# Kernel optimization log

Measured on AMD Instinct MI355X. Metric: run time of the kernel, lower is better.

Reference implementation:

```python
import jax, jax.numpy as jnp
import numpy as np

# dims: H heads, D=word_size (d_model), E=embed_dim per head, N=seq_len=n, K=linformer k
H, D, E, N, K = 16, 1024, 64, 4096, 256


def setup_inputs() -> dict:
    key = jax.random.key(0)
    ks = jax.random.split(key, 9)
    s = 0.02  # init scale for weights
    return {
        "x":  jax.random.normal(ks[0], (N, D), jnp.float32),
        # per-head QKV linears: torch Linear weight is (out=E, in=D), bias (E,)
        "Wq": jax.random.normal(ks[1], (H, E, D), jnp.float32) * s,
        "bq": jnp.zeros((H, E), jnp.float32),
        "Wk": jax.random.normal(ks[2], (H, E, D), jnp.float32) * s,
        "bk": jnp.zeros((H, E), jnp.float32),
        "Wv": jax.random.normal(ks[3], (H, E, D), jnp.float32) * s,
        "bv": jnp.zeros((H, E), jnp.float32),
        # per-head E/F sequence projections: Linear(n=N, k=K) -> weight (K, N), bias (K,)
        "Ew": jax.random.normal(ks[4], (H, K, N), jnp.float32) * s,
        "Eb": jnp.zeros((H, K), jnp.float32),
        "Fw": jax.random.normal(ks[5], (H, K, N), jnp.float32) * s,
        "Fb": jnp.zeros((H, K), jnp.float32),
        # output projection: Linear(H*E, E, bias=False) -> weight (E, H*E)
        "Wo": jax.random.normal(ks[6], (E, H * E), jnp.float32) * s,
    }


def reference(x, Wq, bq, Wk, bk, Wv, bv, Ew, Eb, Fw, Fb, Wo):
    # per-head Q/K/V projections, batched over heads: (H, N, E)
    q = jnp.einsum('nd,hed->hne', x, Wq) + bq[:, None, :]
    k = jnp.einsum('nd,hed->hne', x, Wk) + bk[:, None, :]
    v = jnp.einsum('nd,hed->hne', x, Wv) + bv[:, None, :]
    # low-rank sequence-length projection of K and V: (H, K, E)
    kp = jnp.einsum('hjn,hne->hje', Ew, k) + Eb[:, :, None]
    vp = jnp.einsum('hjn,hne->hje', Fw, v) + Fb[:, :, None]
    # scaled dot-product attention against projected keys: (H, N, K)
    score = jnp.einsum('hne,hje->hnj', q, kp) / jnp.sqrt(jnp.float32(E))
    attn = jax.nn.softmax(score, axis=-1)
    z = jnp.einsum('hnj,hje->hne', attn, vp)  # (H, N, E)
    # concat heads along feature dim (matches torch.cat(dim=1)): (N, H*E)
    zs = jnp.transpose(z, (1, 0, 2)).reshape(N, H * E)
    # final projection Linear(H*E, E, bias=False)
    return zs @ Wo.T  # (N, E)
```

## Files before the change

### kernel.cpp

```cpp
#include <hip/hip_runtime.h>
#include <hip/hip_bf16.h>

typedef __attribute__((ext_vector_type(4))) float f32x4;
typedef __attribute__((ext_vector_type(8))) short s16x8;
typedef __attribute__((ext_vector_type(4))) short s16x4;
typedef unsigned short u16;


__device__ __forceinline__ f32x4 mfma16(s16x8 a, s16x8 b, f32x4 c) {
    return __builtin_amdgcn_mfma_f32_16x16x32_bf16(a, b, c, 0, 0, 0);
}

__device__ __forceinline__ u16 bf(float f) {
    union { float f; unsigned u; } x; x.f = f;
    return (u16)((x.u + 0x7fffu + ((x.u >> 16) & 1u)) >> 16);
}
__device__ __forceinline__ unsigned pkbf(float a, float b) {
    union { float f; unsigned u; } x, y; x.f = a; y.f = b;
    unsigned ra = x.u + 0x7fffu + ((x.u >> 16) & 1u);
    unsigned rb = y.u + 0x7fffu + ((y.u >> 16) & 1u);
    return (ra >> 16) | (rb & 0xffff0000u);
}

__device__ __forceinline__ void gl_lds16(const u16* g, u16* l) {
    __builtin_amdgcn_global_load_lds(
        (const __attribute__((address_space(1))) unsigned*)g,
        (__attribute__((address_space(3))) unsigned*)l, 16, 0, 0);
}


__global__ __launch_bounds__(256) void cvt_all_kernel(
        const float* __restrict__ x,  const float* __restrict__ Wq,
        const float* __restrict__ Wk, const float* __restrict__ Wv,
        const float* __restrict__ Wo,
        u16* __restrict__ xb, u16* __restrict__ wb, u16* __restrict__ wob) {
    int i = blockIdx.x * 256 + threadIdx.x;
    const float* src; u16* dst; int off;
    if (i < 1048576)      { src = x;  dst = xb;            off = i; }
    else if (i < 1310720) { src = Wq; dst = wb;            off = i - 1048576; }
    else if (i < 1572864) { src = Wk; dst = wb + 1048576;  off = i - 1310720; }
    else if (i < 1835008) { src = Wv; dst = wb + 2097152;  off = i - 1572864; }
    else if (i < 1851392) { src = Wo; dst = wob;           off = i - 1835008; }
    else return;
    f32x4 v = ((const f32x4*)src)[off];
    union { s16x4 v; unsigned u[2]; } r;
    r.u[0] = pkbf(v.x, v.y);
    r.u[1] = pkbf(v.z, v.w);
    ((s16x4*)dst)[off] = r.v;
}


__global__ __launch_bounds__(256, 3) void qkv_kernel(
        const u16* __restrict__ xb, const u16* __restrict__ wb,
        const float* __restrict__ bq, const float* __restrict__ bk,
        const float* __restrict__ bv,
        u16* __restrict__ qo, u16* __restrict__ kTo, u16* __restrict__ vTo) {
    __shared__ u16 As[128 * 32];
    __shared__ u16 Bs[128 * 32];
    int bx   = blockIdx.x % 24;
    int by   = blockIdx.x / 24;
    int tid  = threadIdx.x;
    int lane = tid & 63, w = tid >> 6;
    int l15  = lane & 15, quad = lane >> 4;
    int wr   = w >> 1, wc = w & 1;

    const u16* Ag = xb + (size_t)(by * 128 + (tid >> 2)) * 1024 + (tid & 3) * 8;
    const u16* Bg = wb + (size_t)(bx * 128 + (tid >> 2)) * 1024 + (tid & 3) * 8;
    u16* Al = As + tid * 8;
    u16* Bl = Bs + tid * 8;

    const u16* abase = As + (wr * 64 + l15) * 32 + quad * 8;
    const u16* bbase = Bs + (wc * 64 + l15) * 32 + quad * 8;

    f32x4 acc[4][4] = {};
    for (int k0 = 0; k0 < 1024; k0 += 32) {
        gl_lds16(Ag + k0, Al);
        gl_lds16(Ag + 64 * 1024 + k0, Al + 64 * 32);
        gl_lds16(Bg + k0, Bl);
        gl_lds16(Bg + 64 * 1024 + k0, Bl + 64 * 32);
        __syncthreads();
        s16x8 a[4], b[4];
#pragma unroll
        for (int mi = 0; mi < 4; mi++) a[mi] = *(const s16x8*)(abase + mi * 16 * 32);
#pragma unroll
        for (int nj = 0; nj < 4; nj++) b[nj] = *(const s16x8*)(bbase + nj * 16 * 32);
#pragma unroll
        for (int mi = 0; mi < 4; mi++)
#pragma unroll
            for (int nj = 0; nj < 4; nj++) acc[mi][nj] = mfma16(a[mi], b[nj], acc[mi][nj]);
        __syncthreads();
    }

    int fblk = (bx * 128 + wc * 64) >> 6;
    int mat  = fblk >> 4, h = fblk & 15;
    const float* bias = (mat == 0) ? bq : (mat == 1 ? bk : bv);
#pragma unroll
    for (int nj = 0; nj < 4; nj++) {
        int e = nj * 16 + l15;
        float bb = bias[h * 64 + e];
#pragma unroll
        for (int mi = 0; mi < 4; mi++) {
            int n0 = by * 128 + wr * 64 + mi * 16 + quad * 4;
            f32x4 c = acc[mi][nj];
            if (mat == 0) {
                u16* p = qo + ((size_t)h * 4096 + n0) * 64 + e;
#pragma unroll
                for (int r = 0; r < 4; r++) p[(size_t)r * 64] = bf(c[r] + bb);
            } else {
                u16* p = (mat == 1 ? kTo : vTo) + ((size_t)h * 64 + e) * 4096 + n0;
                union { s16x4 v; u16 s[4]; } pk;
#pragma unroll
                for (int r = 0; r < 4; r++) pk.s[r] = bf(c[r] + bb);
                *(s16x4*)p = pk.v;
            }
        }
    }
}


__global__ __launch_bounds__(256, 2) void kpvp_kernel(
        const float* __restrict__ Ew, const float* __restrict__ Fw,
        const u16* __restrict__ kT, const u16* __restrict__ vT,
        float* __restrict__ accs) {
    __shared__ u16 As[256 * 40];
    __shared__ u16 Bs[64 * 32];
    int b    = blockIdx.x;
    int ks   = b & 15, h = (b >> 4) & 15, p = b >> 8;
    int tid  = threadIdx.x;
    int lane = tid & 63, w = tid >> 6;
    int l15  = lane & 15, quad = lane >> 4;

    const float* Ag = (p ? Fw : Ew)
        + (size_t)(h * 256 + (tid >> 3)) * 4096 + ks * 256 + (tid & 7) * 4;
    const u16* Bg = (p ? vT : kT)
        + ((size_t)h * 64 + (tid >> 2)) * 4096 + ks * 256 + (tid & 3) * 8;
    u16* Aw = As + (tid >> 3) * 40 + (tid & 7) * 4;
    u16* Bl = Bs + tid * 8;

    const u16* abase = As + (w * 64 + l15) * 40 + quad * 8;
    const u16* bbase = Bs + l15 * 32 + quad * 8;

    f32x4 acc[4][4] = {};
    for (int s = 0; s < 8; s++) {
        int kk = s * 32;
        gl_lds16(Bg + kk, Bl);
#pragma unroll
        for (int pr = 0; pr < 8; pr++) {
            f32x4 v = *(const f32x4*)(Ag + (size_t)pr * 32 * 4096 + kk);
            union { s16x4 q; unsigned u[2]; } rr;
            rr.u[0] = pkbf(v.x, v.y);
            rr.u[1] = pkbf(v.z, v.w);
            *(s16x4*)(Aw + pr * 32 * 40) = rr.q;
        }
        __syncthreads();
        s16x8 a[4], bb2[4];
#pragma unroll
        for (int mt = 0; mt < 4; mt++) a[mt] = *(const s16x8*)(abase + mt * 16 * 40);
#pragma unroll
        for (int nt = 0; nt < 4; nt++) bb2[nt] = *(const s16x8*)(bbase + nt * 16 * 32);
#pragma unroll
        for (int mt = 0; mt < 4; mt++)
#pragma unroll
            for (int nt = 0; nt < 4; nt++)
                acc[mt][nt] = mfma16(a[mt], bb2[nt], acc[mt][nt]);
        __syncthreads();
    }

    size_t base = (size_t)ks * 524288
        + ((size_t)(p * 16 + h) * 256 + w * 64 + quad * 4) * 64 + l15;
#pragma unroll
    for (int mt = 0; mt < 4; mt++)
#pragma unroll
        for (int nt = 0; nt < 4; nt++)
#pragma unroll
            for (int r = 0; r < 4; r++)
                accs[base + (size_t)(mt * 16 + r) * 64 + nt * 16] = acc[mt][nt][r];
}


__global__ __launch_bounds__(256) void packkv_kernel(
        const float* __restrict__ accs, const float* __restrict__ Eb,
        const float* __restrict__ Fb, u16* __restrict__ kp, u16* __restrict__ vpT) {
    int idx = blockIdx.x * 256 + threadIdx.x;
    float v = 0.f;
#pragma unroll
    for (int s = 0; s < 16; s++) v += accs[idx + (size_t)s * 524288];
    int p = idx >> 18, h = (idx >> 14) & 15, j = (idx >> 6) & 255, e = idx & 63;
    if (p == 0) {
        v += Eb[h * 256 + j];
        kp[((size_t)(h * 256 + j)) * 64 + e] = bf(v * 0.125f);
    } else {
        v += Fb[h * 256 + j];
        vpT[((size_t)(h * 64 + e)) * 256 + j] = bf(v);
    }
}


__global__ __launch_bounds__(256) void attn_kernel(
        const u16* __restrict__ q, const u16* __restrict__ kp,
        const u16* __restrict__ vpT, u16* __restrict__ zs) {
    __shared__ u16 ps[4][16][256];
    int bm   = blockIdx.x & 63, h = blockIdx.x >> 6;
    int lane = threadIdx.x & 63, w = threadIdx.x >> 6;
    int l15  = lane & 15, quad = lane >> 4;
    int nbase = bm * 64 + w * 16;

    f32x4 s[16] = {};
    const u16* qp  = q  + ((size_t)h * 4096 + nbase + l15) * 64 + quad * 8;
    const u16* kpp = kp + ((size_t)h * 256 + l15) * 64 + quad * 8;
#pragma unroll
    for (int e0 = 0; e0 < 64; e0 += 32) {
        s16x8 a = *(const s16x8*)(qp + e0);
#pragma unroll
        for (int jt = 0; jt < 16; jt++) {
            s16x8 b = *(const s16x8*)(kpp + jt * 16 * 64 + e0);
            s[jt] = mfma16(a, b, s[jt]);
        }
    }

    float lsum[4];
#pragma unroll
    for (int r = 0; r < 4; r++) {
        float m = s[0][r];
#pragma unroll
        for (int jt = 1; jt < 16; jt++) m = fmaxf(m, s[jt][r]);
        m = fmaxf(m, __shfl_xor(m, 1));
        m = fmaxf(m, __shfl_xor(m, 2));
        m = fmaxf(m, __shfl_xor(m, 4));
        m = fmaxf(m, __shfl_xor(m, 8));
        float l = 0.f;
#pragma unroll
        for (int jt = 0; jt < 16; jt++) {
            float pv = __expf(s[jt][r] - m);
            s[jt][r] = pv;
            l += pv;
        }
        l += __shfl_xor(l, 1);
        l += __shfl_xor(l, 2);
        l += __shfl_xor(l, 4);
        l += __shfl_xor(l, 8);
        lsum[r] = l;
    }

#pragma unroll
    for (int jt = 0; jt < 16; jt++)
#pragma unroll
        for (int r = 0; r < 4; r++)
            ps[w][quad * 4 + r][jt * 16 + l15] = bf(s[jt][r]);
    __syncthreads();

    f32x4 z[4] = {};
    const u16* vp = vpT + ((size_t)h * 64 + l15) * 256 + quad * 8;
#pragma unroll
    for (int kj = 0; kj < 8; kj++) {
        s16x8 a = *(const s16x8*)&ps[w][l15][kj * 32 + quad * 8];
#pragma unroll
        for (int et = 0; et < 4; et++) {
            s16x8 b = *(const s16x8*)(vp + et * 16 * 256 + kj * 32);
            z[et] = mfma16(a, b, z[et]);
        }
    }
#pragma unroll
    for (int et = 0; et < 4; et++) {
        int e = et * 16 + l15;
        u16* o = zs + ((size_t)(nbase + quad * 4)) * 1024 + h * 64 + e;
#pragma unroll
        for (int r = 0; r < 4; r++) o[(size_t)r * 1024] = bf(z[et][r] / lsum[r]);
    }
}


__global__ __launch_bounds__(256) void out_kernel(
        const u16* __restrict__ zs, const u16* __restrict__ wob,
        float* __restrict__ oslice) {
    int ks   = blockIdx.x & 3;
    int bm   = blockIdx.x >> 2;
    int lane = threadIdx.x & 63, w = threadIdx.x >> 6;
    int l15  = lane & 15, quad = lane >> 4;
    int row0 = bm * 128 + w * 32;

    const u16* A = zs  + (size_t)(row0 + l15) * 1024 + ks * 256 + quad * 8;
    const u16* B = wob + (size_t)l15 * 1024 + ks * 256 + quad * 8;

    f32x4 acc[2][4] = {};
    for (int k = 0; k < 256; k += 32) {
        s16x8 a0 = *(const s16x8*)(A + k);
        s16x8 a1 = *(const s16x8*)(A + 16 * 1024 + k);
#pragma unroll
        for (int nt = 0; nt < 4; nt++) {
            s16x8 bv = *(const s16x8*)(B + (size_t)nt * 16 * 1024 + k);
            acc[0][nt] = mfma16(a0, bv, acc[0][nt]);
            acc[1][nt] = mfma16(a1, bv, acc[1][nt]);
        }
    }
    float* os = oslice + (size_t)ks * 262144;
#pragma unroll
    for (int mt = 0; mt < 2; mt++)
#pragma unroll
        for (int nt = 0; nt < 4; nt++) {
            int e = nt * 16 + l15;
            int n0 = row0 + mt * 16 + quad * 4;
            float* o = os + (size_t)n0 * 64 + e;
#pragma unroll
            for (int r = 0; r < 4; r++) o[(size_t)r * 64] = acc[mt][nt][r];
        }
}

__global__ __launch_bounds__(256) void outred_kernel(
        const float* __restrict__ oslice, float* __restrict__ out) {
    int i = blockIdx.x * 256 + threadIdx.x;
    out[i] = oslice[i] + oslice[i + 262144] + oslice[i + 524288] + oslice[i + 786432];
}


extern "C" void kernel_launch(void* const* d_in, const int* in_sizes, int n_in,
                              void* d_out, int out_size, void* d_ws, size_t ws_size,
                              hipStream_t stream) {
    const float* x  = (const float*)d_in[0];
    const float* Wq = (const float*)d_in[1];
    const float* bq = (const float*)d_in[2];
    const float* Wk = (const float*)d_in[3];
    const float* bk = (const float*)d_in[4];
    const float* Wv = (const float*)d_in[5];
    const float* bv = (const float*)d_in[6];
    const float* Ew = (const float*)d_in[7];
    const float* Eb = (const float*)d_in[8];
    const float* Fw = (const float*)d_in[9];
    const float* Fb = (const float*)d_in[10];
    const float* Wo = (const float*)d_in[11];

    char* ws = (char*)d_ws;
    u16*   qb   = (u16*)(ws + 0);
    u16*   kT   = (u16*)(ws + 8388608);
    u16*   vT   = (u16*)(ws + 16777216);
    u16*   zsb  = (u16*)(ws + 25165824);
    float* accs = (float*)(ws + 33554432);
    u16*   kp   = (u16*)(ws + 67108864);
    u16*   vpT  = (u16*)(ws + 67633152);
    u16*   xb   = (u16*)(ws + 68157440);
    u16*   wb   = (u16*)(ws + 76546048);
    u16*   wob  = (u16*)(ws + 82837504);

    cvt_all_kernel<<<7232, 256, 0, stream>>>(x, Wq, Wk, Wv, Wo, xb, wb, wob);
    qkv_kernel<<<768, 256, 0, stream>>>(xb, wb, bq, bk, bv, qb, kT, vT);
    kpvp_kernel<<<512, 256, 0, stream>>>(Ew, Fw, kT, vT, accs);
    packkv_kernel<<<2048, 256, 0, stream>>>(accs, Eb, Fb, kp, vpT);
    attn_kernel<<<1024, 256, 0, stream>>>(qb, kp, vpT, zsb);
    out_kernel<<<128, 256, 0, stream>>>(zsb, wob, (float*)accs);
    outred_kernel<<<1024, 256, 0, stream>>>((const float*)accs, (float*)d_out);
}
```

Baseline: 299.4 us.

## Retile kpvp into two launches, vectorize packkv, keep attention probs in registers

The kpvp GEMM now covers half of the K rows per block, with a 2x2 wave layout and a higher occupancy bound, and is split into two launches over the split-K halves. packkv now reads vectorized fp32 partials and transposes vp through LDS so its stores are coalesced. The attention kernel swaps the MFMA operand order so each lane holds a full score column. The softmax reduction then needs only cross-quad shuffles, and the bf16 probabilities feed a K=16 MFMA straight from registers with no LDS round-trip. The normalization moves before the PV product, which shifts where bf16 rounding happens, and the extra launch adds some overhead.

```diff
diff --git a/kernel.cpp b/kernel.cpp
--- a/kernel.cpp
+++ b/kernel.cpp
@@ -9,6 +9,16 @@
 
 __device__ __forceinline__ f32x4 mfma16(s16x8 a, s16x8 b, f32x4 c) {
     return __builtin_amdgcn_mfma_f32_16x16x32_bf16(a, b, c, 0, 0, 0);
+}
+
+__device__ __forceinline__ f32x4 mfma_k16(s16x4 a, s16x4 b, f32x4 c) {
+#if __has_builtin(__builtin_amdgcn_mfma_f32_16x16x16bf16_1k)
+    return __builtin_amdgcn_mfma_f32_16x16x16bf16_1k(a, b, c, 0, 0, 0);
+#else
+    s16x8 a8 = { a[0], a[1], a[2], a[3], 0, 0, 0, 0 };
+    s16x8 b8 = { b[0], b[1], b[2], b[3], 0, 0, 0, 0 };
+    return __builtin_amdgcn_mfma_f32_16x16x32_bf16(a8, b8, c, 0, 0, 0);
+#endif
 }
 
 __device__ __forceinline__ u16 bf(float f) {
@@ -118,34 +128,35 @@
 }
 
 
-__global__ __launch_bounds__(256, 2) void kpvp_kernel(
+__global__ __launch_bounds__(256, 4) void kpvp_kernel(
         const float* __restrict__ Ew, const float* __restrict__ Fw,
         const u16* __restrict__ kT, const u16* __restrict__ vT,
-        float* __restrict__ accs) {
-    __shared__ u16 As[256 * 40];
+        float* __restrict__ accs, int ks0) {
+    __shared__ u16 As[128 * 40];
     __shared__ u16 Bs[64 * 32];
     int b    = blockIdx.x;
-    int ks   = b & 15, h = (b >> 4) & 15, p = b >> 8;
+    int ks   = (b & 7) + ks0, jt = (b >> 3) & 1, h = (b >> 4) & 15, p = b >> 8;
     int tid  = threadIdx.x;
     int lane = tid & 63, w = tid >> 6;
     int l15  = lane & 15, quad = lane >> 4;
+    int wm   = w & 1, wn = w >> 1;
 
     const float* Ag = (p ? Fw : Ew)
-        + (size_t)(h * 256 + (tid >> 3)) * 4096 + ks * 256 + (tid & 7) * 4;
+        + (size_t)(h * 256 + jt * 128 + (tid >> 3)) * 4096 + ks * 256 + (tid & 7) * 4;
     const u16* Bg = (p ? vT : kT)
         + ((size_t)h * 64 + (tid >> 2)) * 4096 + ks * 256 + (tid & 3) * 8;
     u16* Aw = As + (tid >> 3) * 40 + (tid & 7) * 4;
     u16* Bl = Bs + tid * 8;
 
-    const u16* abase = As + (w * 64 + l15) * 40 + quad * 8;
-    const u16* bbase = Bs + l15 * 32 + quad * 8;
-
-    f32x4 acc[4][4] = {};
+    const u16* abase = As + (wm * 64 + l15) * 40 + quad * 8;
+    const u16* bbase = Bs + (wn * 32 + l15) * 32 + quad * 8;
+
+    f32x4 acc[4][2] = {};
     for (int s = 0; s < 8; s++) {
         int kk = s * 32;
         gl_lds16(Bg + kk, Bl);
 #pragma unroll
-        for (int pr = 0; pr < 8; pr++) {
+        for (int pr = 0; pr < 4; pr++) {
             f32x4 v = *(const f32x4*)(Ag + (size_t)pr * 32 * 4096 + kk);
             union { s16x4 q; unsigned u[2]; } rr;
             rr.u[0] = pkbf(v.x, v.y);
@@ -153,25 +164,26 @@
             *(s16x4*)(Aw + pr * 32 * 40) = rr.q;
         }
         __syncthreads();
-        s16x8 a[4], bb2[4];
+        s16x8 a[4], bb2[2];
 #pragma unroll
         for (int mt = 0; mt < 4; mt++) a[mt] = *(const s16x8*)(abase + mt * 16 * 40);
 #pragma unroll
-        for (int nt = 0; nt < 4; nt++) bb2[nt] = *(const s16x8*)(bbase + nt * 16 * 32);
+        for (int nt = 0; nt < 2; nt++) bb2[nt] = *(const s16x8*)(bbase + nt * 16 * 32);
 #pragma unroll
         for (int mt = 0; mt < 4; mt++)
 #pragma unroll
-            for (int nt = 0; nt < 4; nt++)
+            for (int nt = 0; nt < 2; nt++)
                 acc[mt][nt] = mfma16(a[mt], bb2[nt], acc[mt][nt]);
         __syncthreads();
     }
 
     size_t base = (size_t)ks * 524288
-        + ((size_t)(p * 16 + h) * 256 + w * 64 + quad * 4) * 64 + l15;
+        + ((size_t)(p * 16 + h) * 256 + jt * 128 + wm * 64 + quad * 4) * 64
+        + wn * 32 + l15;
 #pragma unroll
     for (int mt = 0; mt < 4; mt++)
 #pragma unroll
-        for (int nt = 0; nt < 4; nt++)
+        for (int nt = 0; nt < 2; nt++)
 #pragma unroll
             for (int r = 0; r < 4; r++)
                 accs[base + (size_t)(mt * 16 + r) * 64 + nt * 16] = acc[mt][nt][r];
@@ -181,17 +193,38 @@
 __global__ __launch_bounds__(256) void packkv_kernel(
         const float* __restrict__ accs, const float* __restrict__ Eb,
         const float* __restrict__ Fb, u16* __restrict__ kp, u16* __restrict__ vpT) {
-    int idx = blockIdx.x * 256 + threadIdx.x;
-    float v = 0.f;
-#pragma unroll
-    for (int s = 0; s < 16; s++) v += accs[idx + (size_t)s * 524288];
-    int p = idx >> 18, h = (idx >> 14) & 15, j = (idx >> 6) & 255, e = idx & 63;
+    __shared__ u16 tile[32 * 72];
+    int b  = blockIdx.x;
+    int p  = b >> 7, h = (b >> 3) & 15, j0 = (b & 7) * 32;
+    int t  = threadIdx.x;
+    int jr = t >> 3, ec = (t & 7) * 8;
+
+    size_t base = ((size_t)(p * 16 + h) * 256 + j0 + jr) * 64 + ec;
+    float v[8] = {};
+#pragma unroll
+    for (int s = 0; s < 16; s++) {
+        f32x4 lo = *(const f32x4*)(accs + base + (size_t)s * 524288);
+        f32x4 hi = *(const f32x4*)(accs + base + (size_t)s * 524288 + 4);
+#pragma unroll
+        for (int i = 0; i < 4; i++) { v[i] += lo[i]; v[i + 4] += hi[i]; }
+    }
+    float bias = p ? Fb[h * 256 + j0 + jr] : Eb[h * 256 + j0 + jr];
+    float scale = p ? 1.0f : 0.125f;
+    union { s16x8 o; unsigned u[4]; } pk;
+#pragma unroll
+    for (int i = 0; i < 4; i++)
+        pk.u[i] = pkbf((v[2 * i] + bias) * scale, (v[2 * i + 1] + bias) * scale);
+
     if (p == 0) {
-        v += Eb[h * 256 + j];
-        kp[((size_t)(h * 256 + j)) * 64 + e] = bf(v * 0.125f);
+        *(s16x8*)(kp + ((size_t)(h * 256 + j0 + jr)) * 64 + ec) = pk.o;
     } else {
-        v += Fb[h * 256 + j];
-        vpT[((size_t)(h * 64 + e)) * 256 + j] = bf(v);
+        *(s16x8*)(tile + jr * 72 + ec) = pk.o;
+        __syncthreads();
+        int er = t >> 2, jc = (t & 3) * 8;
+        union { s16x8 o; u16 s[8]; } tr;
+#pragma unroll
+        for (int i = 0; i < 8; i++) tr.s[i] = tile[(jc + i) * 72 + er];
+        *(s16x8*)(vpT + ((size_t)(h * 64 + er)) * 256 + j0 + jc) = tr.o;
     }
 }
 
@@ -199,7 +232,6 @@
 __global__ __launch_bounds__(256) void attn_kernel(
         const u16* __restrict__ q, const u16* __restrict__ kp,
         const u16* __restrict__ vpT, u16* __restrict__ zs) {
-    __shared__ u16 ps[4][16][256];
     int bm   = blockIdx.x & 63, h = blockIdx.x >> 6;
     int lane = threadIdx.x & 63, w = threadIdx.x >> 6;
     int l15  = lane & 15, quad = lane >> 4;
@@ -210,62 +242,54 @@
     const u16* kpp = kp + ((size_t)h * 256 + l15) * 64 + quad * 8;
 #pragma unroll
     for (int e0 = 0; e0 < 64; e0 += 32) {
-        s16x8 a = *(const s16x8*)(qp + e0);
+        s16x8 bq = *(const s16x8*)(qp + e0);
 #pragma unroll
         for (int jt = 0; jt < 16; jt++) {
-            s16x8 b = *(const s16x8*)(kpp + jt * 16 * 64 + e0);
-            s[jt] = mfma16(a, b, s[jt]);
-        }
-    }
-
-    float lsum[4];
-#pragma unroll
-    for (int r = 0; r < 4; r++) {
-        float m = s[0][r];
-#pragma unroll
-        for (int jt = 1; jt < 16; jt++) m = fmaxf(m, s[jt][r]);
-        m = fmaxf(m, __shfl_xor(m, 1));
-        m = fmaxf(m, __shfl_xor(m, 2));
-        m = fmaxf(m, __shfl_xor(m, 4));
-        m = fmaxf(m, __shfl_xor(m, 8));
-        float l = 0.f;
-#pragma unroll
-        for (int jt = 0; jt < 16; jt++) {
+            s16x8 aq = *(const s16x8*)(kpp + jt * 16 * 64 + e0);
+            s[jt] = mfma16(aq, bq, s[jt]);
+        }
+    }
+
+    float m = s[0][0];
+#pragma unroll
+    for (int jt = 0; jt < 16; jt++)
+#pragma unroll
+        for (int r = 0; r < 4; r++) m = fmaxf(m, s[jt][r]);
+    m = fmaxf(m, __shfl_xor(m, 16));
+    m = fmaxf(m, __shfl_xor(m, 32));
+    float l = 0.f;
+#pragma unroll
+    for (int jt = 0; jt < 16; jt++)
+#pragma unroll
+        for (int r = 0; r < 4; r++) {
             float pv = __expf(s[jt][r] - m);
             s[jt][r] = pv;
             l += pv;
         }
-        l += __shfl_xor(l, 1);
-        l += __shfl_xor(l, 2);
-        l += __shfl_xor(l, 4);
-        l += __shfl_xor(l, 8);
-        lsum[r] = l;
-    }
-
-#pragma unroll
-    for (int jt = 0; jt < 16; jt++)
-#pragma unroll
-        for (int r = 0; r < 4; r++)
-            ps[w][quad * 4 + r][jt * 16 + l15] = bf(s[jt][r]);
-    __syncthreads();
+    l += __shfl_xor(l, 16);
+    l += __shfl_xor(l, 32);
+    float inv = 1.0f / l;
 
     f32x4 z[4] = {};
-    const u16* vp = vpT + ((size_t)h * 64 + l15) * 256 + quad * 8;
-#pragma unroll
-    for (int kj = 0; kj < 8; kj++) {
-        s16x8 a = *(const s16x8*)&ps[w][l15][kj * 32 + quad * 8];
+    const u16* vb = vpT + (size_t)h * 64 * 256 + l15 * 256 + quad * 4;
+#pragma unroll
+    for (int jt = 0; jt < 16; jt++) {
+        union { s16x4 v; unsigned u[2]; } a;
+        a.u[0] = pkbf(s[jt][0] * inv, s[jt][1] * inv);
+        a.u[1] = pkbf(s[jt][2] * inv, s[jt][3] * inv);
 #pragma unroll
         for (int et = 0; et < 4; et++) {
-            s16x8 b = *(const s16x8*)(vp + et * 16 * 256 + kj * 32);
-            z[et] = mfma16(a, b, z[et]);
-        }
-    }
+            s16x4 bv = *(const s16x4*)(vb + (size_t)et * 16 * 256 + jt * 16);
+            z[et] = mfma_k16(a.v, bv, z[et]);
+        }
+    }
+
 #pragma unroll
     for (int et = 0; et < 4; et++) {
         int e = et * 16 + l15;
         u16* o = zs + ((size_t)(nbase + quad * 4)) * 1024 + h * 64 + e;
 #pragma unroll
-        for (int r = 0; r < 4; r++) o[(size_t)r * 1024] = bf(z[et][r] / lsum[r]);
+        for (int r = 0; r < 4; r++) o[(size_t)r * 1024] = bf(z[et][r]);
     }
 }
 
@@ -343,8 +367,9 @@
 
     cvt_all_kernel<<<7232, 256, 0, stream>>>(x, Wq, Wk, Wv, Wo, xb, wb, wob);
     qkv_kernel<<<768, 256, 0, stream>>>(xb, wb, bq, bk, bv, qb, kT, vT);
-    kpvp_kernel<<<512, 256, 0, stream>>>(Ew, Fw, kT, vT, accs);
-    packkv_kernel<<<2048, 256, 0, stream>>>(accs, Eb, Fb, kp, vpT);
+    kpvp_kernel<<<512, 256, 0, stream>>>(Ew, Fw, kT, vT, accs, 0);
+    kpvp_kernel<<<512, 256, 0, stream>>>(Ew, Fw, kT, vT, accs, 8);
+    packkv_kernel<<<256, 256, 0, stream>>>(accs, Eb, Fb, kp, vpT);
     attn_kernel<<<1024, 256, 0, stream>>>(qb, kp, vpT, zsb);
     out_kernel<<<128, 256, 0, stream>>>(zsb, wob, (float*)accs);
     outred_kernel<<<1024, 256, 0, stream>>>((const float*)accs, (float*)d_out);
```

Result: no change. 304.1 us (+1.6%).
